# Kernel tuning notes

Measured on AMD Instinct MI355X. Metric: run time of the kernel, lower is better.

## Reference

```python
import jax, jax.numpy as jnp
import numpy as np

LN2 = float(np.log(2.0))
CUTOFF_L = 0.5


def _ssp(x):
    # shifted softplus: log(0.5*exp(x) + 0.5)
    return jax.nn.softplus(x) - LN2


def _pair_idx(n):
    # ordered pairs arranged [n, n-1]: for each i, all j != i
    idx = np.arange(n)
    j = np.stack([np.concatenate([idx[:k], idx[k + 1:]]) for k in range(n)])  # [n, n-1]
    i = np.broadcast_to(idx[:, None], j.shape)
    return jnp.asarray(i), jnp.asarray(j)


def _mlp3(x, w1, b1, w2, b2, w3, b3):
    h = _ssp(x @ w1 + b1)
    h = _ssp(h @ w2 + b2)
    return h @ w3 + b3


def _backflow_cutoff(r, L=CUTOFF_L):
    r = r / L
    return jnp.where(r < L, r ** 2 * (6.0 - 8.0 * r + 3.0 * r ** 2), jnp.ones((), r.dtype))


def setup_inputs() -> dict:
    key = jax.random.key(0)
    ks = jax.random.split(key, 12)
    B, N, D, K = 512, 32, 256, 8
    dims_e = [D, 40, 6, 1]
    dims_n = [D, 81, 25, 8]

    def lin(k, fi, fo):
        return jax.random.normal(k, (fi, fo), jnp.float32) / np.sqrt(fi)

    inp = {
        'rs': jax.random.normal(ks[0], (B, N, 3), jnp.float32),
        'xs': jax.random.normal(ks[1], (B, N, D), jnp.float32),
        'coords': jax.random.normal(ks[2], (K, 3), jnp.float32) * 2.0,
        'ew1': lin(ks[3], dims_e[0], dims_e[1]), 'eb1': jnp.zeros((dims_e[1],), jnp.float32),
        'ew2': lin(ks[4], dims_e[1], dims_e[2]), 'eb2': jnp.zeros((dims_e[2],), jnp.float32),
        'ew3': lin(ks[5], dims_e[2], dims_e[3]), 'eb3': jnp.zeros((dims_e[3],), jnp.float32),
        'nw1': lin(ks[6], dims_n[0], dims_n[1]), 'nb1': jnp.zeros((dims_n[1],), jnp.float32),
        'nw2': lin(ks[7], dims_n[1], dims_n[2]), 'nb2': jnp.zeros((dims_n[2],), jnp.float32),
        'nw3': lin(ks[8], dims_n[2], dims_n[3]), 'nb3': jnp.zeros((dims_n[3],), jnp.float32),
    }
    return inp


def reference(rs, xs, coords, ew1, eb1, ew2, eb2, ew3, eb3,
              nw1, nb1, nw2, nb2, nw3, nb3):
    n_elec = rs.shape[-2]
    i, j = _pair_idx(n_elec)  # [n, n-1] static index arrays

    # electron-electron backflow
    diffs_elec = rs[..., i, :] - rs[..., j, :]                    # [B, n, n-1, 3]
    pair_feat = xs[..., i, :] * xs[..., j, :]                     # [B, n, n-1, D]
    w_pair = _mlp3(pair_feat, ew1, eb1, ew2, eb2, ew3, eb3)       # [B, n, n-1, 1]
    bf_elec = (w_pair * diffs_elec).sum(axis=-2)                  # [B, n, 3]

    # electron-nucleus backflow
    diffs_nuc = rs[..., :, None, :] - coords                      # [B, n, K, 3]
    w_nuc = _mlp3(xs, nw1, nb1, nw2, nb2, nw3, nb3)               # [B, n, K]
    bf_nuc = (w_nuc[..., None] * diffs_nuc).sum(axis=-2)          # [B, n, 3]

    dist_nuc = jnp.linalg.norm(diffs_nuc, axis=-1)                # [B, n, K]
    cutoff = _backflow_cutoff(dist_nuc).prod(axis=-1)             # [B, n]

    return rs + 1e-4 * cutoff[..., None] * (bf_elec + bf_nuc)
```

## Files before the change

### kernel.cpp

```cpp
#include <hip/hip_runtime.h>
#include <stdint.h>

static constexpr int B_ = 512, N_ = 32, D_ = 256, K_ = 8;
static constexpr int E1 = 40, E2 = 6;
static constexpr int N1 = 81, N2 = 25, N3 = 8;
static constexpr int XBP = 264;
static constexpr int H1P = 72;
static constexpr int HEP = 88;
static constexpr int EWT = 264;
static constexpr int TKP = 44;
static constexpr float LN2f  = 0.69314718055994530942f;
static constexpr float L2Ef  = 1.44269504088896340736f;

typedef float    f32x4 __attribute__((ext_vector_type(4)));
typedef _Float16 f16x8 __attribute__((ext_vector_type(8)));
typedef _Float16 f16x4 __attribute__((ext_vector_type(4)));

__device__ __forceinline__ float sspf(float x) {
    float t = __builtin_amdgcn_exp2f(x * L2Ef);
    return LN2f * __builtin_amdgcn_logf(fmaf(t, 0.5f, 0.5f));
}

__global__ __launch_bounds__(512) void k_fused(
    const float* __restrict__ rs, const float* __restrict__ xs,
    const float* __restrict__ coords,
    const float* __restrict__ ew1, const float* __restrict__ eb1,
    const float* __restrict__ ew2, const float* __restrict__ eb2,
    const float* __restrict__ ew3, const float* __restrict__ eb3,
    const float* __restrict__ nw1, const float* __restrict__ nb1,
    const float* __restrict__ nw2, const float* __restrict__ nb2,
    const float* __restrict__ nw3, const float* __restrict__ nb3,
    float* __restrict__ out)
{
    __shared__ alignas(16) _Float16 xs_h[N_ * XBP];
    __shared__ alignas(16) _Float16 wbuf[E1 * EWT];
    __shared__ alignas(16) char uni[8 * 16 * H1P * 2];
    __shared__ float nw2_s[N1 * N2];
    __shared__ float nw3_s[N2 * N3];
    __shared__ float rs_s[N_ * 3];
    __shared__ float nb2_s[N2];
    __shared__ float nb3_s[N3];
    __shared__ float co_s[K_ * 3];
    __shared__ float bfn_s[N_ * 3];
    __shared__ float cut_s[N_];
    __shared__ float bfe_s[N_ * 3];

    _Float16* h1e = (_Float16*)uni;
    float*    h2e = (float*)(uni + N_ * HEP * 2);

    const int b = blockIdx.x, t = threadIdx.x;
    const int wv = t >> 6, l = t & 63, quad = l >> 4, c = l & 15;

    f16x8 b2f[2];
    #pragma unroll
    for (int Kt = 0; Kt < 2; ++Kt) {
        union { uint32_t d[4]; f16x8 v; } f;
        #pragma unroll
        for (int d2 = 0; d2 < 4; ++d2) {
            int k0 = Kt * 32 + quad * 8 + 2 * d2;
            union { _Float16 h[2]; uint32_t u; } pk;
            pk.h[0] = (_Float16)((k0 < E1 && c < E2) ? ew2[k0 * E2 + c] : 0.f);
            pk.h[1] = (_Float16)((k0 + 1 < E1 && c < E2) ? ew2[(k0 + 1) * E2 + c] : 0.f);
            f.d[d2] = pk.u;
        }
        b2f[Kt] = f.v;
    }
    float eb1v[3];
    #pragma unroll
    for (int Nt = 0; Nt < 3; ++Nt) { int n = Nt * 16 + c; eb1v[Nt] = (n < E1) ? eb1[n] : 0.f; }
    const float eb2v = (c < E2) ? eb2[c] : 0.f;
    const float w3v  = (c < E2) ? ew3[c] : 0.f;
    const float eb3v = eb3[0];
    float nb1v[2];
    #pragma unroll
    for (int e = 0; e < 2; ++e) {
        int p = wv + 8 * e, n = (p >> 1) * 16 + c;
        nb1v[e] = (p < 12 && n < N1) ? nb1[n] : 0.f;
    }

    {
        const float4* src = (const float4*)(xs + (size_t)b * N_ * D_);
        #pragma unroll
        for (int u = 0; u < 4; ++u) {
            int q = t + 512 * u;
            float4 v = src[q];
            int row = q >> 6, col4 = q & 63;
            union { _Float16 h[4]; uint64_t u64; } pk;
            pk.h[0] = (_Float16)v.x; pk.h[1] = (_Float16)v.y;
            pk.h[2] = (_Float16)v.z; pk.h[3] = (_Float16)v.w;
            *(uint64_t*)&xs_h[row * XBP + col4 * 4] = pk.u64;
        }
    }
    {
        const float4* src = (const float4*)ew1;
        #pragma unroll
        for (int u = 0; u < 5; ++u) {
            int q = t + 512 * u;
            float4 v = src[q];
            int k = q / 10, n0 = (q - 10 * k) * 4;
            wbuf[(n0 + 0) * EWT + k] = (_Float16)v.x;
            wbuf[(n0 + 1) * EWT + k] = (_Float16)v.y;
            wbuf[(n0 + 2) * EWT + k] = (_Float16)v.z;
            wbuf[(n0 + 3) * EWT + k] = (_Float16)v.w;
        }
    }
    if (t < N_ * 3) rs_s[t] = rs[b * N_ * 3 + t];
    for (int i2 = t; i2 < N1 * N2; i2 += 512) nw2_s[i2] = nw2[i2];
    if (t < N2 * N3) nw3_s[t] = nw3[t];
    if (t < N2) nb2_s[t] = nb2[t];
    if (t < N3) nb3_s[t] = nb3[t];
    if (t < K_ * 3) co_s[t] = coords[t];
    __syncthreads();

    f16x8 b1f[3][8];
    #pragma unroll
    for (int Nt = 0; Nt < 3; ++Nt) {
        int n = Nt * 16 + c;
        bool ok = (n < E1);
        int row = ok ? n : 0;
        #pragma unroll
        for (int Kt = 0; Kt < 8; ++Kt) {
            f16x8 v = *(const f16x8*)&wbuf[row * EWT + Kt * 32 + quad * 8];
            if (!ok) v = (f16x8)(_Float16)0.f;
            b1f[Nt][Kt] = v;
        }
    }

    float pf[6];
    #pragma unroll
    for (int u = 0; u < 6; ++u) {
        int idx = t + 512 * u;
        int k = idx / 96, n = idx - 96 * k;
        pf[u] = (n < N1) ? nw1[k * N1 + n] : 0.f;
    }
    __syncthreads();

    {
        f32x4 acc3[2];
        #pragma unroll
        for (int e = 0; e < 2; ++e) acc3[e] = (f32x4){0.f, 0.f, 0.f, 0.f};

        #pragma unroll 1
        for (int Kt = 0; Kt < 8; ++Kt) {
            _Float16* dst = wbuf + (Kt & 1) * (96 * TKP);
            #pragma unroll
            for (int u = 0; u < 6; ++u) {
                int idx = t + 512 * u;
                int k = idx / 96, n = idx - 96 * k;
                int ks = k ^ (((n >> 4) & 1) << 3);
                dst[n * TKP + ks] = (_Float16)pf[u];
            }
            if (Kt < 7) {
                const float* wk = nw1 + ((Kt + 1) * 32) * N1;
                #pragma unroll
                for (int u = 0; u < 6; ++u) {
                    int idx = t + 512 * u;
                    int k = idx / 96, n = idx - 96 * k;
                    pf[u] = (n < N1) ? wk[k * N1 + n] : 0.f;
                }
            }
            __syncthreads();
            const _Float16* T = wbuf + (Kt & 1) * (96 * TKP);
            #pragma unroll
            for (int e = 0; e < 2; ++e) {
                int p = wv + 8 * e;
                if (p < 12) {
                    int Mt = p & 1, Nt = p >> 1;
                    f16x8 A = *(const f16x8*)&xs_h[(Mt * 16 + c) * XBP + Kt * 32 + quad * 8];
                    int rb = (Nt * 16 + c) * TKP;
                    int kb = (quad * 8) ^ ((Nt & 1) << 3);
                    f16x4 lo = *(const f16x4*)&T[rb + kb];
                    f16x4 hi = *(const f16x4*)&T[rb + kb + 4];
                    f16x8 Bf = __builtin_shufflevector(lo, hi, 0, 1, 2, 3, 4, 5, 6, 7);
                    acc3[e] = __builtin_amdgcn_mfma_f32_16x16x32_f16(A, Bf, acc3[e], 0, 0, 0);
                }
            }
        }
        __syncthreads();
        #pragma unroll
        for (int e = 0; e < 2; ++e) {
            int p = wv + 8 * e;
            if (p < 12) {
                int Mt = p & 1, Nt = p >> 1;
                int n = Nt * 16 + c;
                if (n < N1) {
                    #pragma unroll
                    for (int r2 = 0; r2 < 4; ++r2) {
                        int m = Mt * 16 + quad * 4 + r2;
                        h1e[m * HEP + n] = (_Float16)sspf(acc3[e][r2] + nb1v[e]);
                    }
                }
            }
        }
    }
    __syncthreads();

    {
        const int r = t >> 4, s = t & 15;
        const int n0 = 2 * s;
        if (n0 < N2) {
            float a0 = 0.f, a1 = 0.f;
            const int rb = r * HEP;
            for (int kk = 0; kk < N1; ++kk) {
                float hv = (float)h1e[rb + kk];
                const float* wrow = nw2_s + kk * N2 + n0;
                a0 = fmaf(hv, wrow[0], a0);
                if (n0 + 1 < N2) a1 = fmaf(hv, wrow[1], a1);
            }
            h2e[r * 26 + n0] = sspf(a0 + nb2_s[n0]);
            if (n0 + 1 < N2) h2e[r * 26 + n0 + 1] = sspf(a1 + nb2_s[n0 + 1]);
        }
    }
    __syncthreads();

    if (t < 256) {
        const int r = t >> 3, s = t & 7;
        float w = nb3_s[s];
        const int rb = r * 26;
        #pragma unroll
        for (int kk = 0; kk < N2; ++kk)
            w = fmaf(h2e[rb + kk], nw3_s[kk * N3 + s], w);

        float dx = rs_s[r * 3 + 0] - co_s[s * 3 + 0];
        float dy = rs_s[r * 3 + 1] - co_s[s * 3 + 1];
        float dz = rs_s[r * 3 + 2] - co_s[s * 3 + 2];
        float cx = w * dx, cy = w * dy, cz = w * dz;
        #pragma unroll
        for (int m2 = 1; m2 < 8; m2 <<= 1) {
            cx += __shfl_xor(cx, m2);
            cy += __shfl_xor(cy, m2);
            cz += __shfl_xor(cz, m2);
        }
        float rr  = sqrtf(dx * dx + dy * dy + dz * dz);
        float xsc = 2.f * rr;
        float cf  = (xsc < 0.5f) ? xsc * xsc * (6.f - 8.f * xsc + 3.f * xsc * xsc) : 1.f;
        #pragma unroll
        for (int m2 = 1; m2 < 8; m2 <<= 1) cf *= __shfl_xor(cf, m2);
        if (s == 0) {
            bfn_s[r * 3 + 0] = cx;
            bfn_s[r * 3 + 1] = cy;
            bfn_s[r * 3 + 2] = cz;
            cut_s[r] = cf;
        }
    }
    __syncthreads();

    _Float16* myh1 = (_Float16*)(uni + wv * (16 * H1P * 2));
    *(uint64_t*)&myh1[c * H1P + 48 + quad * 4] = 0ull;

    #pragma unroll 1
    for (int q8 = 0; q8 < 4; ++q8) {
        const int i = wv + 8 * q8;
        f32x4 acc[2][3];
        #pragma unroll
        for (int h = 0; h < 2; ++h)
            #pragma unroll
            for (int Nt = 0; Nt < 3; ++Nt) acc[h][Nt] = (f32x4){0.f, 0.f, 0.f, 0.f};

        #pragma unroll
        for (int Kt = 0; Kt < 8; ++Kt) {
            const int koff = Kt * 32 + quad * 8;
            f16x8 iv  = *(const f16x8*)&xs_h[i * XBP + koff];
            f16x8 jv0 = *(const f16x8*)&xs_h[c * XBP + koff];
            f16x8 jv1 = *(const f16x8*)&xs_h[(16 + c) * XBP + koff];
            f16x8 A0 = iv * jv0;
            f16x8 A1 = iv * jv1;
            #pragma unroll
            for (int Nt = 0; Nt < 3; ++Nt) {
                acc[0][Nt] = __builtin_amdgcn_mfma_f32_16x16x32_f16(A0, b1f[Nt][Kt], acc[0][Nt], 0, 0, 0);
                acc[1][Nt] = __builtin_amdgcn_mfma_f32_16x16x32_f16(A1, b1f[Nt][Kt], acc[1][Nt], 0, 0, 0);
            }
        }

        const float rix = rs_s[i * 3 + 0], riy = rs_s[i * 3 + 1], riz = rs_s[i * 3 + 2];
        float cxi = 0.f, cyi = 0.f, czi = 0.f;
        #pragma unroll
        for (int h = 0; h < 2; ++h) {
            #pragma unroll
            for (int Nt = 0; Nt < 3; ++Nt) {
                #pragma unroll
                for (int r2 = 0; r2 < 4; ++r2) {
                    float hv = sspf(acc[h][Nt][r2] + eb1v[Nt]);
                    myh1[(quad * 4 + r2) * H1P + Nt * 16 + c] = (_Float16)hv;
                }
            }
            f32x4 acc2 = {0.f, 0.f, 0.f, 0.f};
            #pragma unroll
            for (int Kt2 = 0; Kt2 < 2; ++Kt2) {
                f16x8 a2 = *(const f16x8*)&myh1[c * H1P + Kt2 * 32 + quad * 8];
                acc2 = __builtin_amdgcn_mfma_f32_16x16x32_f16(a2, b2f[Kt2], acc2, 0, 0, 0);
            }
            float wp[4];
            #pragma unroll
            for (int r2 = 0; r2 < 4; ++r2) wp[r2] = sspf(acc2[r2] + eb2v) * w3v;
            #pragma unroll
            for (int m2 = 1; m2 < 16; m2 <<= 1) {
                #pragma unroll
                for (int r2 = 0; r2 < 4; ++r2) wp[r2] += __shfl_xor(wp[r2], m2);
            }
            #pragma unroll
            for (int r2 = 0; r2 < 4; ++r2) {
                int j = quad * 4 + r2 + 16 * h;
                float wj = wp[r2] + eb3v;
                cxi = fmaf(wj, rix - rs_s[j * 3 + 0], cxi);
                cyi = fmaf(wj, riy - rs_s[j * 3 + 1], cyi);
                czi = fmaf(wj, riz - rs_s[j * 3 + 2], czi);
            }
        }
        #pragma unroll
        for (int m2 = 16; m2 < 64; m2 <<= 1) {
            cxi += __shfl_xor(cxi, m2);
            cyi += __shfl_xor(cyi, m2);
            czi += __shfl_xor(czi, m2);
        }
        if (l == 0) {
            bfe_s[i * 3 + 0] = cxi;
            bfe_s[i * 3 + 1] = cyi;
            bfe_s[i * 3 + 2] = czi;
        }
    }
    __syncthreads();

    if (t < N_ * 3) {
        int i = t / 3;
        out[(size_t)b * (N_ * 3) + t] =
            rs_s[t] + 1e-4f * cut_s[i] * (bfe_s[t] + bfn_s[t]);
    }
}

extern "C" void kernel_launch(void* const* d_in, const int* in_sizes, int n_in,
                              void* d_out, int out_size, void* d_ws, size_t ws_size,
                              hipStream_t stream)
{
    const float* rs     = (const float*)d_in[0];
    const float* xs     = (const float*)d_in[1];
    const float* coords = (const float*)d_in[2];
    const float* ew1    = (const float*)d_in[3];
    const float* eb1    = (const float*)d_in[4];
    const float* ew2    = (const float*)d_in[5];
    const float* eb2    = (const float*)d_in[6];
    const float* ew3    = (const float*)d_in[7];
    const float* eb3    = (const float*)d_in[8];
    const float* nw1    = (const float*)d_in[9];
    const float* nb1    = (const float*)d_in[10];
    const float* nw2    = (const float*)d_in[11];
    const float* nb2    = (const float*)d_in[12];
    const float* nw3    = (const float*)d_in[13];
    const float* nb3    = (const float*)d_in[14];

    k_fused<<<B_, 512, 0, stream>>>(rs, xs, coords, ew1, eb1, ew2, eb2, ew3, eb3,
                                    nw1, nb1, nw2, nb2, nw3, nb3, (float*)d_out);
}
```

Baseline: 146.6 us.

## Restructure nuclear MLP layer 1 per-wave and move layer 2 onto MFMA

The first nuclear MLP layer is reorganized so each of six waves stages its own 16-column fp16 weight tile, with no block-wide barriers inside the K loop. The block-level double-buffered tile and the eight __syncthreads it needed are removed. The second layer (81->25) moves from scalar FMA loops over fp32 shared weights to 16x16x32 fp16 MFMA, using a transposed, padded fp16 copy of nw2 and zeroed h1 padding. This lowers synchronization and scalar ALU work, but rounds layer-2 inputs and weights to fp16 and leaves fewer waves busy in layer 1.

```diff
diff --git a/kernel.cpp b/kernel.cpp
--- a/kernel.cpp
+++ b/kernel.cpp
@@ -6,15 +6,16 @@
 static constexpr int N1 = 81, N2 = 25, N3 = 8;
 static constexpr int XBP = 264;
 static constexpr int H1P = 72;
-static constexpr int HEP = 88;
+static constexpr int HEP = 96;
 static constexpr int EWT = 264;
-static constexpr int TKP = 44;
+static constexpr int TKP = 48;
+static constexpr int NWP = 104;
+static constexpr int TILE16 = 16 * TKP;
 static constexpr float LN2f  = 0.69314718055994530942f;
 static constexpr float L2Ef  = 1.44269504088896340736f;
 
 typedef float    f32x4 __attribute__((ext_vector_type(4)));
 typedef _Float16 f16x8 __attribute__((ext_vector_type(8)));
-typedef _Float16 f16x4 __attribute__((ext_vector_type(4)));
 
 __device__ __forceinline__ float sspf(float x) {
     float t = __builtin_amdgcn_exp2f(x * L2Ef);
@@ -34,8 +35,7 @@
 {
     __shared__ alignas(16) _Float16 xs_h[N_ * XBP];
     __shared__ alignas(16) _Float16 wbuf[E1 * EWT];
-    __shared__ alignas(16) char uni[8 * 16 * H1P * 2];
-    __shared__ float nw2_s[N1 * N2];
+    __shared__ alignas(16) char uni[18688];
     __shared__ float nw3_s[N2 * N3];
     __shared__ float rs_s[N_ * 3];
     __shared__ float nb2_s[N2];
@@ -45,8 +45,9 @@
     __shared__ float cut_s[N_];
     __shared__ float bfe_s[N_ * 3];
 
-    _Float16* h1e = (_Float16*)uni;
-    float*    h2e = (float*)(uni + N_ * HEP * 2);
+    _Float16* h1e  = (_Float16*)(uni + 9216);
+    float*    h2e  = (float*)(uni + 15360);
+    _Float16* nw2T = (_Float16*)uni;
 
     const int b = blockIdx.x, t = threadIdx.x;
     const int wv = t >> 6, l = t & 63, quad = l >> 4, c = l & 15;
@@ -71,12 +72,6 @@
     const float eb2v = (c < E2) ? eb2[c] : 0.f;
     const float w3v  = (c < E2) ? ew3[c] : 0.f;
     const float eb3v = eb3[0];
-    float nb1v[2];
-    #pragma unroll
-    for (int e = 0; e < 2; ++e) {
-        int p = wv + 8 * e, n = (p >> 1) * 16 + c;
-        nb1v[e] = (p < 12 && n < N1) ? nb1[n] : 0.f;
-    }
 
     {
         const float4* src = (const float4*)(xs + (size_t)b * N_ * D_);
@@ -104,12 +99,62 @@
             wbuf[(n0 + 3) * EWT + k] = (_Float16)v.w;
         }
     }
+    if (t < 128) {
+        int m = t >> 2, q4 = t & 3;
+        *(uint64_t*)(uni + 9216 + m * (HEP * 2) + 160 + q4 * 8) = 0ull;
+    }
     if (t < N_ * 3) rs_s[t] = rs[b * N_ * 3 + t];
-    for (int i2 = t; i2 < N1 * N2; i2 += 512) nw2_s[i2] = nw2[i2];
     if (t < N2 * N3) nw3_s[t] = nw3[t];
     if (t < N2) nb2_s[t] = nb2[t];
     if (t < N3) nb3_s[t] = nb3[t];
     if (t < K_ * 3) co_s[t] = coords[t];
+    __syncthreads();
+
+    if (wv < 6) {
+        _Float16* tile = (_Float16*)uni + wv * TILE16;
+        const int ln = l & 15, lq = l >> 4;
+        const int gn = wv * 16 + ln;
+        const bool gok = (gn < N1);
+        const int n_col = wv * 16 + c;
+        const float nb1v = (n_col < N1) ? nb1[n_col] : 0.f;
+
+        float pf[8];
+        #pragma unroll
+        for (int u = 0; u < 8; ++u)
+            pf[u] = gok ? nw1[(lq + 4 * u) * N1 + gn] : 0.f;
+
+        f32x4 acc[2];
+        acc[0] = (f32x4){0.f, 0.f, 0.f, 0.f};
+        acc[1] = (f32x4){0.f, 0.f, 0.f, 0.f};
+
+        #pragma unroll 1
+        for (int Kt = 0; Kt < 8; ++Kt) {
+            #pragma unroll
+            for (int u = 0; u < 8; ++u)
+                tile[ln * TKP + lq + 4 * u] = (_Float16)pf[u];
+            if (Kt < 7) {
+                const float* wk = nw1 + (Kt + 1) * 32 * N1 + gn;
+                #pragma unroll
+                for (int u = 0; u < 8; ++u)
+                    pf[u] = gok ? wk[(lq + 4 * u) * N1] : 0.f;
+            }
+            f16x8 Bf = *(const f16x8*)&tile[c * TKP + quad * 8];
+            #pragma unroll
+            for (int Mt = 0; Mt < 2; ++Mt) {
+                f16x8 A = *(const f16x8*)&xs_h[(Mt * 16 + c) * XBP + Kt * 32 + quad * 8];
+                acc[Mt] = __builtin_amdgcn_mfma_f32_16x16x32_f16(A, Bf, acc[Mt], 0, 0, 0);
+            }
+        }
+        if (n_col < N1) {
+            #pragma unroll
+            for (int Mt = 0; Mt < 2; ++Mt)
+                #pragma unroll
+                for (int r2 = 0; r2 < 4; ++r2) {
+                    int m = Mt * 16 + quad * 4 + r2;
+                    h1e[m * HEP + n_col] = (_Float16)sspf(acc[Mt][r2] + nb1v);
+                }
+        }
+    }
     __syncthreads();
 
     f16x8 b1f[3][8];
@@ -125,90 +170,31 @@
             b1f[Nt][Kt] = v;
         }
     }
-
-    float pf[6];
     #pragma unroll
     for (int u = 0; u < 6; ++u) {
         int idx = t + 512 * u;
-        int k = idx / 96, n = idx - 96 * k;
-        pf[u] = (n < N1) ? nw1[k * N1 + n] : 0.f;
-    }
-    __syncthreads();
-
-    {
-        f32x4 acc3[2];
-        #pragma unroll
-        for (int e = 0; e < 2; ++e) acc3[e] = (f32x4){0.f, 0.f, 0.f, 0.f};
-
-        #pragma unroll 1
-        for (int Kt = 0; Kt < 8; ++Kt) {
-            _Float16* dst = wbuf + (Kt & 1) * (96 * TKP);
-            #pragma unroll
-            for (int u = 0; u < 6; ++u) {
-                int idx = t + 512 * u;
-                int k = idx / 96, n = idx - 96 * k;
-                int ks = k ^ (((n >> 4) & 1) << 3);
-                dst[n * TKP + ks] = (_Float16)pf[u];
-            }
-            if (Kt < 7) {
-                const float* wk = nw1 + ((Kt + 1) * 32) * N1;
-                #pragma unroll
-                for (int u = 0; u < 6; ++u) {
-                    int idx = t + 512 * u;
-                    int k = idx / 96, n = idx - 96 * k;
-                    pf[u] = (n < N1) ? wk[k * N1 + n] : 0.f;
-                }
-            }
-            __syncthreads();
-            const _Float16* T = wbuf + (Kt & 1) * (96 * TKP);
-            #pragma unroll
-            for (int e = 0; e < 2; ++e) {
-                int p = wv + 8 * e;
-                if (p < 12) {
-                    int Mt = p & 1, Nt = p >> 1;
-                    f16x8 A = *(const f16x8*)&xs_h[(Mt * 16 + c) * XBP + Kt * 32 + quad * 8];
-                    int rb = (Nt * 16 + c) * TKP;
-                    int kb = (quad * 8) ^ ((Nt & 1) << 3);
-                    f16x4 lo = *(const f16x4*)&T[rb + kb];
-                    f16x4 hi = *(const f16x4*)&T[rb + kb + 4];
-                    f16x8 Bf = __builtin_shufflevector(lo, hi, 0, 1, 2, 3, 4, 5, 6, 7);
-                    acc3[e] = __builtin_amdgcn_mfma_f32_16x16x32_f16(A, Bf, acc3[e], 0, 0, 0);
-                }
-            }
-        }
-        __syncthreads();
-        #pragma unroll
-        for (int e = 0; e < 2; ++e) {
-            int p = wv + 8 * e;
-            if (p < 12) {
-                int Mt = p & 1, Nt = p >> 1;
-                int n = Nt * 16 + c;
-                if (n < N1) {
-                    #pragma unroll
-                    for (int r2 = 0; r2 < 4; ++r2) {
-                        int m = Mt * 16 + quad * 4 + r2;
-                        h1e[m * HEP + n] = (_Float16)sspf(acc3[e][r2] + nb1v[e]);
-                    }
-                }
-            }
-        }
-    }
-    __syncthreads();
-
-    {
-        const int r = t >> 4, s = t & 15;
-        const int n0 = 2 * s;
-        if (n0 < N2) {
-            float a0 = 0.f, a1 = 0.f;
-            const int rb = r * HEP;
-            for (int kk = 0; kk < N1; ++kk) {
-                float hv = (float)h1e[rb + kk];
-                const float* wrow = nw2_s + kk * N2 + n0;
-                a0 = fmaf(hv, wrow[0], a0);
-                if (n0 + 1 < N2) a1 = fmaf(hv, wrow[1], a1);
-            }
-            h2e[r * 26 + n0] = sspf(a0 + nb2_s[n0]);
-            if (n0 + 1 < N2) h2e[r * 26 + n0 + 1] = sspf(a1 + nb2_s[n0 + 1]);
+        int n = idx / 96, kk = idx - 96 * n;
+        float v = (kk < N1 && n < N2) ? nw2[kk * N2 + n] : 0.f;
+        nw2T[n * NWP + kk] = (_Float16)v;
+    }
+    __syncthreads();
+
+    if (wv < 4) {
+        const int Mt = wv & 1, Nt = wv >> 1;
+        f32x4 acc2 = {0.f, 0.f, 0.f, 0.f};
+        #pragma unroll
+        for (int Kt2 = 0; Kt2 < 3; ++Kt2) {
+            f16x8 A  = *(const f16x8*)&h1e[(Mt * 16 + c) * HEP + Kt2 * 32 + quad * 8];
+            f16x8 Bf = *(const f16x8*)&nw2T[(Nt * 16 + c) * NWP + Kt2 * 32 + quad * 8];
+            acc2 = __builtin_amdgcn_mfma_f32_16x16x32_f16(A, Bf, acc2, 0, 0, 0);
+        }
+        int n = Nt * 16 + c;
+        if (n < N2) {
+            #pragma unroll
+            for (int r2 = 0; r2 < 4; ++r2) {
+                int m = Mt * 16 + quad * 4 + r2;
+                h2e[m * 26 + n] = sspf(acc2[r2] + nb2_s[n]);
+            }
         }
     }
     __syncthreads();
```

Measured after the change: 133.8 us. 8.7% less time.
